# Kernel tuning notes

Hardware: AMD Instinct MI355X
Metric: run time of the kernel (lower is better)

## Reference

```python
import jax, jax.numpy as jnp
import numpy as np

N = 100000   # nodes
E = 600000   # edges
F_IN = 128   # input feature dim
H = 256      # hidden_channels


def setup_inputs() -> dict:
    key = jax.random.key(0)
    ks = jax.random.split(key, 8)
    x = jax.random.normal(ks[0], (N, F_IN), dtype=jnp.float32)
    edge_index = jax.random.randint(ks[1], (2, E), 0, N, dtype=jnp.int64)
    # SAGEConv params: out = lin_l(mean_agg) + lin_r(x_root); bias only on lin_l (PyG default)
    s1 = 1.0 / np.sqrt(F_IN)
    s2 = 1.0 / np.sqrt(H)
    Wl1 = jax.random.uniform(ks[2], (F_IN, H), jnp.float32, -s1, s1)
    Wr1 = jax.random.uniform(ks[3], (F_IN, H), jnp.float32, -s1, s1)
    b1 = jnp.zeros((H,), jnp.float32)
    Wl2 = jax.random.uniform(ks[4], (H, H), jnp.float32, -s2, s2)
    Wr2 = jax.random.uniform(ks[5], (H, H), jnp.float32, -s2, s2)
    b2 = jnp.zeros((H,), jnp.float32)
    return {"x": x, "edge_index": edge_index, "Wl1": Wl1, "Wr1": Wr1, "b1": b1,
            "Wl2": Wl2, "Wr2": Wr2, "b2": b2}


def _sage_conv(h, src, dst, Wl, Wr, b):
    # mean aggregation of source-node features at destination nodes
    msg = h[src]                                             # [E, d]
    agg = jax.ops.segment_sum(msg, dst, num_segments=N)      # [N, d]
    cnt = jax.ops.segment_sum(jnp.ones((src.shape[0],), h.dtype), dst, num_segments=N)
    agg = agg / jnp.maximum(cnt, 1.0)[:, None]
    return agg @ Wl + b + h @ Wr


def reference(x, edge_index, Wl1, Wr1, b1, Wl2, Wr2, b2):
    src, dst = edge_index[0], edge_index[1]
    h = jax.nn.relu(_sage_conv(x, src, dst, Wl1, Wr1, b1))
    return _sage_conv(h, src, dst, Wl2, Wr2, b2)
```

## Files before the change

### kernel.cpp

```cpp
#include <hip/hip_runtime.h>

#define Nn 100000
#define Ee 600000
#define Fin 128
#define Hd  256
#define NB  ((Nn + 1023) / 1024)

typedef __attribute__((ext_vector_type(8))) short short8;
typedef __attribute__((ext_vector_type(4))) float floatx4;

__device__ __forceinline__ float bf2f(unsigned short h) {
    return __uint_as_float(((unsigned int)h) << 16);
}
__device__ __forceinline__ unsigned short f2bf(float f) {
    unsigned int u = __float_as_uint(f);
    u += 0x7FFFu + ((u >> 16) & 1u);
    return (unsigned short)(u >> 16);
}
__device__ __forceinline__ float loadf(const void* p, int i, int f32) {
    return f32 ? ((const float*)p)[i] : bf2f(((const unsigned short*)p)[i]);
}
__device__ __forceinline__ void gload_lds16(const void* g, void* lds) {
    __builtin_amdgcn_global_load_lds((const __attribute__((address_space(1))) void*)g,
                                     (__attribute__((address_space(3))) void*)lds,
                                     16, 0, 0);
}

__global__ void k_detect(const unsigned int* __restrict__ ei,
                         const unsigned short* __restrict__ xu,
                         int* __restrict__ flag) {
    if (blockIdx.x == 0 && threadIdx.x == 0) {
        int is64 = 1;
        for (int i = 1; i < 64; i += 2)
            if (ei[i] != 0u) { is64 = 0; break; }
        flag[0] = is64;
        int isf32 = 0;
        for (int i = 0; i < 512; i += 2) {
            unsigned e = (xu[i] >> 7) & 0xFFu;
            if (e >= 0xC0u) { isf32 = 1; break; }
        }
        flag[1] = isf32;
    }
}

__device__ __forceinline__ void get_edge(const int* __restrict__ ei, int is64, int e,
                                         int& s, int& d) {
    if (is64) { s = ei[2 * e]; d = ei[2 * (Ee + e)]; }
    else      { s = ei[e];     d = ei[Ee + e]; }
}

__global__ void k_zero(int* __restrict__ p, int n) {
    int i = blockIdx.x * 256 + threadIdx.x;
    if (i < n) p[i] = 0;
}

__global__ void k_convert(const void* __restrict__ x, unsigned short* __restrict__ xb,
                          const int* __restrict__ flag) {
    int i = (blockIdx.x * 256 + threadIdx.x) * 4;
    if (i >= Nn * Fin) return;
    if (flag[1]) {
        float4 v = ((const float4*)x)[i >> 2];
        ushort4 u;
        u.x = f2bf(v.x); u.y = f2bf(v.y); u.z = f2bf(v.z); u.w = f2bf(v.w);
        ((ushort4*)xb)[i >> 2] = u;
    } else {
        ((ushort4*)xb)[i >> 2] = ((const ushort4*)x)[i >> 2];
    }
}

__global__ void k_prep(const void* __restrict__ Wl1, const void* __restrict__ Wr1,
                       const void* __restrict__ Wl2, const void* __restrict__ Wr2,
                       unsigned short* __restrict__ Wt1, unsigned short* __restrict__ Wt2,
                       const int* __restrict__ flag) {
    int f32 = flag[1];
    int tid = blockIdx.x * 256 + threadIdx.x;
    if (tid < 256 * 256) {
        int n = tid >> 8, k = tid & 255;
        float v = (k < 128) ? loadf(Wl1, k * 256 + n, f32) : loadf(Wr1, (k - 128) * 256 + n, f32);
        Wt1[n * 256 + k] = f2bf(v);
    }
    int t2 = tid - 256 * 256;
    if (t2 >= 0 && t2 < 256 * 512) {
        int n = t2 >> 9, k = t2 & 511;
        float v = (k < 256) ? loadf(Wl2, k * 256 + n, f32) : loadf(Wr2, (k - 256) * 256 + n, f32);
        Wt2[n * 512 + k] = f2bf(v);
    }
}

__global__ void k_count(const int* __restrict__ ei, const int* __restrict__ flag,
                        int* __restrict__ cnt) {
    int e = blockIdx.x * 256 + threadIdx.x;
    if (e >= Ee) return;
    int is64 = flag[0], s, d;
    get_edge(ei, is64, e, s, d);
    atomicAdd(&cnt[d], 1);
}

__global__ void k_bsum(const int* __restrict__ cnt, int* __restrict__ bsum) {
    __shared__ int red[256];
    int b = blockIdx.x, t = threadIdx.x;
    int i = b * 1024 + t * 4;
    int s = 0;
    if (i + 3 < Nn) {
        int4 v = *reinterpret_cast<const int4*>(cnt + i);
        s = v.x + v.y + v.z + v.w;
    } else {
        for (int j = 0; j < 4; j++) if (i + j < Nn) s += cnt[i + j];
    }
    red[t] = s;
    __syncthreads();
    for (int off = 128; off > 0; off >>= 1) {
        if (t < off) red[t] += red[t + off];
        __syncthreads();
    }
    if (t == 0) bsum[b] = red[0];
}

__global__ void k_bscan(const int* __restrict__ bsum, int* __restrict__ bpre,
                        int* __restrict__ rowptr) {
    __shared__ int sc[128];
    int t = threadIdx.x;
    int v = (t < NB) ? bsum[t] : 0;
    sc[t] = v;
    __syncthreads();
    for (int off = 1; off < 128; off <<= 1) {
        int add = (t >= off) ? sc[t - off] : 0;
        __syncthreads();
        sc[t] += add;
        __syncthreads();
    }
    if (t < NB) bpre[t] = sc[t] - v;
    if (t == 127) rowptr[Nn] = sc[127];
}

__global__ void k_rowptr(const int* __restrict__ cnt, const int* __restrict__ bpre,
                         int* __restrict__ rowptr) {
    __shared__ int sc[256];
    int b = blockIdx.x, t = threadIdx.x;
    int i = b * 1024 + t * 4;
    int4 c = make_int4(0, 0, 0, 0);
    if (i + 3 < Nn) {
        c = *reinterpret_cast<const int4*>(cnt + i);
    } else {
        if (i     < Nn) c.x = cnt[i];
        if (i + 1 < Nn) c.y = cnt[i + 1];
        if (i + 2 < Nn) c.z = cnt[i + 2];
        if (i + 3 < Nn) c.w = cnt[i + 3];
    }
    int s = c.x + c.y + c.z + c.w;
    sc[t] = s;
    __syncthreads();
    for (int off = 1; off < 256; off <<= 1) {
        int add = (t >= off) ? sc[t - off] : 0;
        __syncthreads();
        sc[t] += add;
        __syncthreads();
    }
    int p = bpre[b] + sc[t] - s;
    int4 r;
    r.x = p;
    r.y = r.x + c.x;
    r.z = r.y + c.y;
    r.w = r.z + c.z;
    if (i + 3 < Nn) {
        *reinterpret_cast<int4*>(rowptr + i) = r;
    } else {
        if (i     < Nn) rowptr[i]     = r.x;
        if (i + 1 < Nn) rowptr[i + 1] = r.y;
        if (i + 2 < Nn) rowptr[i + 2] = r.z;
        if (i + 3 < Nn) rowptr[i + 3] = r.w;
    }
}

__global__ void k_fill(const int* __restrict__ ei, const int* __restrict__ flag,
                       const int* __restrict__ rowptr, int* __restrict__ cur,
                       int* __restrict__ srcl) {
    int e = blockIdx.x * 256 + threadIdx.x;
    if (e >= Ee) return;
    int is64 = flag[0], s, d;
    get_edge(ei, is64, e, s, d);
    int pos = atomicAdd(&cur[d], 1);
    srcl[rowptr[d] + pos] = s;
}

template <int F, int SIN, int SOUT>
__device__ __forceinline__ void agg_body(const unsigned short* __restrict__ X,
                                         unsigned short* __restrict__ O,
                                         const int* __restrict__ rowptr,
                                         const int* __restrict__ srcl) {
    int gw = (blockIdx.x * blockDim.x + threadIdx.x) >> 6;
    int lane = threadIdx.x & 63;
    if (gw >= Nn) return;
    int b = rowptr[gw], e = rowptr[gw + 1];
    constexpr int C = F / 64;
    float acc[C] = {};
    if (e > b) {
        int last = e - 1;
        for (int i = b; i < e; i += 4) {
            int sv[4];
            float w[4];
#pragma unroll
            for (int j = 0; j < 4; j++) {
                int id = i + j;
                sv[j] = srcl[id < last ? id : last];
                w[j] = (id < e) ? 1.f : 0.f;
            }
            if constexpr (C == 2) {
                ushort2 u[4];
#pragma unroll
                for (int j = 0; j < 4; j++)
                    u[j] = *reinterpret_cast<const ushort2*>(X + (size_t)sv[j] * SIN + lane * 2);
#pragma unroll
                for (int j = 0; j < 4; j++) {
                    acc[0] = fmaf(w[j], bf2f(u[j].x), acc[0]);
                    acc[1] = fmaf(w[j], bf2f(u[j].y), acc[1]);
                }
            } else {
                ushort4 u[4];
#pragma unroll
                for (int j = 0; j < 4; j++)
                    u[j] = *reinterpret_cast<const ushort4*>(X + (size_t)sv[j] * SIN + lane * 4);
#pragma unroll
                for (int j = 0; j < 4; j++) {
                    acc[0] = fmaf(w[j], bf2f(u[j].x), acc[0]);
                    acc[1] = fmaf(w[j], bf2f(u[j].y), acc[1]);
                    acc[2] = fmaf(w[j], bf2f(u[j].z), acc[2]);
                    acc[3] = fmaf(w[j], bf2f(u[j].w), acc[3]);
                }
            }
        }
    }
    float inv = 1.f / (float)max(e - b, 1);
    unsigned short* op = O + (size_t)gw * SOUT + lane * C;
    if constexpr (C == 2) {
        ushort2 u; u.x = f2bf(acc[0] * inv); u.y = f2bf(acc[1] * inv);
        *reinterpret_cast<ushort2*>(op) = u;
    } else {
        ushort4 u;
        u.x = f2bf(acc[0] * inv); u.y = f2bf(acc[1] * inv);
        u.z = f2bf(acc[2] * inv); u.w = f2bf(acc[3] * inv);
        *reinterpret_cast<ushort4*>(op) = u;
    }
}

__global__ void k_agg1(const unsigned short* __restrict__ xb, unsigned short* __restrict__ agg1,
                       const int* __restrict__ rowptr, const int* __restrict__ srcl) {
    agg_body<Fin, Fin, Fin>(xb, agg1, rowptr, srcl);
}

__global__ void k_agg2(const int* __restrict__ rowptr, const int* __restrict__ srcl,
                       const int* __restrict__ flag, unsigned short* __restrict__ acat_ws,
                       void* __restrict__ out) {
    unsigned short* Acat = flag[1] ? (unsigned short*)out : acat_ws;
    agg_body<Hd, 512, 512>(Acat + 256, Acat, rowptr, srcl);
}

template <int KT, int K1, int S1, int S2>
__device__ __forceinline__ void gemm_core_lds(const unsigned short* __restrict__ A1,
                                              const unsigned short* __restrict__ A2,
                                              const unsigned short* __restrict__ Wt,
                                              floatx4 (&acc)[4][4],
                                              unsigned short* sA, unsigned short* sB,
                                              int m_base) {
    const int tid = threadIdx.x;
    const int lane = tid & 63, wid = tid >> 6;
    const int wm = wid & 1, wn = wid >> 1;
    const int quad = lane >> 4, l16 = lane & 15;
    const int n_base = wn * 64;
    const int rs = tid >> 3;
    const int cs = tid & 7;

    for (int kb = 0; kb < KT; kb += 64) {
        __syncthreads();
#pragma unroll
        for (int i = 0; i < 2; i++) {
            int r = i * 64 + rs;
            int gk = kb + ((cs ^ (r & 7)) << 3);
            int m = m_base + r; if (m >= Nn) m = Nn - 1;
            const unsigned short* gp = (gk < K1)
                ? A1 + (size_t)m * S1 + gk
                : A2 + (size_t)m * S2 + (gk - K1);
            gload_lds16(gp, sA + i * 4096 + wid * 512);
        }
#pragma unroll
        for (int i = 0; i < 4; i++) {
            int n = i * 64 + rs;
            int gk = kb + ((cs ^ (n & 7)) << 3);
            gload_lds16(Wt + (size_t)n * KT + gk, sB + i * 4096 + wid * 512);
        }
        __syncthreads();
#pragma unroll
        for (int ks = 0; ks < 64; ks += 32) {
            short8 a[4], b[4];
            int q = (ks >> 3) + quad;
#pragma unroll
            for (int mt = 0; mt < 4; mt++) {
                int r = wm * 64 + mt * 16 + l16;
                a[mt] = *reinterpret_cast<const short8*>(
                    sA + r * 64 + ((q ^ (l16 & 7)) << 3));
            }
#pragma unroll
            for (int nt = 0; nt < 4; nt++) {
                int n = n_base + nt * 16 + l16;
                b[nt] = *reinterpret_cast<const short8*>(
                    sB + n * 64 + ((q ^ (l16 & 7)) << 3));
            }
#pragma unroll
            for (int mt = 0; mt < 4; mt++)
#pragma unroll
                for (int nt = 0; nt < 4; nt++)
                    acc[mt][nt] = __builtin_amdgcn_mfma_f32_16x16x32_bf16(a[mt], b[nt], acc[mt][nt], 0, 0, 0);
        }
    }
}

__global__ __launch_bounds__(512) void k_gemm1(const unsigned short* __restrict__ agg1,
                                               const unsigned short* __restrict__ xb,
                                               const unsigned short* __restrict__ Wt1,
                                               const void* __restrict__ bias,
                                               const int* __restrict__ flag,
                                               unsigned short* __restrict__ acat_ws,
                                               void* __restrict__ out) {
    __shared__ unsigned short sA[8192];
    __shared__ unsigned short sB[16384];
    int f32 = flag[1];
    unsigned short* Acat = f32 ? (unsigned short*)out : acat_ws;
    int wid = threadIdx.x >> 6, lane = threadIdx.x & 63;
    int wm = wid & 1, wn = wid >> 1;
    int quad = lane >> 4, l16 = lane & 15;
    int m_base = blockIdx.x * 128;
    floatx4 acc[4][4] = {};
    gemm_core_lds<256, 128, 128, 128>(agg1, xb, Wt1, acc, sA, sB, m_base);
#pragma unroll
    for (int nt = 0; nt < 4; nt++) {
        int n = wn * 64 + nt * 16 + l16;
        float bv = loadf(bias, n, f32);
#pragma unroll
        for (int mt = 0; mt < 4; mt++) {
#pragma unroll
            for (int r = 0; r < 4; r++) {
                int m = m_base + wm * 64 + mt * 16 + quad * 4 + r;
                if (m < Nn) {
                    float v = acc[mt][nt][r] + bv;
                    v = v > 0.f ? v : 0.f;
                    Acat[(size_t)m * 512 + 256 + n] = f2bf(v);
                }
            }
        }
    }
}

__global__ __launch_bounds__(512) void k_gemm2(const unsigned short* __restrict__ Wt2,
                                               const void* __restrict__ bias,
                                               const int* __restrict__ flag,
                                               unsigned short* __restrict__ acat_ws,
                                               void* __restrict__ out) {
    __shared__ unsigned short sA[8192];
    __shared__ unsigned short sB[16384];
    int f32 = flag[1];
    unsigned short* Acat = f32 ? (unsigned short*)out : acat_ws;
    int wid = threadIdx.x >> 6, lane = threadIdx.x & 63;
    int wm = wid & 1, wn = wid >> 1;
    int quad = lane >> 4, l16 = lane & 15;
    int m_base = blockIdx.x * 128;
    floatx4 acc[4][4] = {};
    gemm_core_lds<512, 256, 512, 512>(Acat, Acat + 256, Wt2, acc, sA, sB, m_base);
    __syncthreads();
#pragma unroll
    for (int nt = 0; nt < 4; nt++) {
        int n = wn * 64 + nt * 16 + l16;
        float bv = loadf(bias, n, f32);
#pragma unroll
        for (int mt = 0; mt < 4; mt++) {
#pragma unroll
            for (int r = 0; r < 4; r++) {
                int m = m_base + wm * 64 + mt * 16 + quad * 4 + r;
                if (m < Nn) {
                    float v = acc[mt][nt][r] + bv;
                    if (f32) ((float*)out)[(size_t)m * Hd + n] = v;
                    else     ((unsigned short*)out)[(size_t)m * Hd + n] = f2bf(v);
                }
            }
        }
    }
}

extern "C" void kernel_launch(void* const* d_in, const int* in_sizes, int n_in,
                              void* d_out, int out_size, void* d_ws, size_t ws_size,
                              hipStream_t stream) {
    const void* x   = d_in[0];
    const int*  ei  = (const int*)d_in[1];
    const void* Wl1 = d_in[2];
    const void* Wr1 = d_in[3];
    const void* b1  = d_in[4];
    const void* Wl2 = d_in[5];
    const void* Wr2 = d_in[6];
    const void* b2  = d_in[7];

    char* ws = (char*)d_ws;
    size_t off_cnt    = 0;
    size_t off_cur    = off_cnt + (size_t)Nn * 4;
    size_t off_rowptr = off_cur + (size_t)Nn * 4;
    size_t off_srcl   = off_rowptr + (size_t)(Nn + 4) * 4;
    size_t off_flag   = off_srcl + (size_t)Ee * 4;
    size_t off_bsum   = ((off_flag + 8 + 255) / 256) * 256;
    size_t off_bpre   = off_bsum + 128 * 4;
    size_t off_wt1    = off_bpre + 128 * 4;
    size_t off_wt2    = off_wt1 + 256 * 256 * 2;
    size_t off_xb     = off_wt2 + 256 * 512 * 2;
    size_t off_agg1   = off_xb + (size_t)Nn * Fin * 2;
    size_t off_acat   = off_agg1 + (size_t)Nn * Fin * 2;

    int*            cnt     = (int*)(ws + off_cnt);
    int*            cur     = (int*)(ws + off_cur);
    int*            rowptr  = (int*)(ws + off_rowptr);
    int*            srcl    = (int*)(ws + off_srcl);
    int*            flag    = (int*)(ws + off_flag);
    int*            bsum    = (int*)(ws + off_bsum);
    int*            bpre    = (int*)(ws + off_bpre);
    unsigned short* Wt1     = (unsigned short*)(ws + off_wt1);
    unsigned short* Wt2     = (unsigned short*)(ws + off_wt2);
    unsigned short* xb      = (unsigned short*)(ws + off_xb);
    unsigned short* agg1    = (unsigned short*)(ws + off_agg1);
    unsigned short* acat_ws = (unsigned short*)(ws + off_acat);

    k_detect<<<1, 64, 0, stream>>>((const unsigned int*)ei, (const unsigned short*)x, flag);
    k_zero<<<(2 * Nn + 255) / 256, 256, 0, stream>>>(cnt, 2 * Nn);
    k_convert<<<(Nn * Fin / 4 + 255) / 256, 256, 0, stream>>>(x, xb, flag);
    k_prep<<<768, 256, 0, stream>>>(Wl1, Wr1, Wl2, Wr2, Wt1, Wt2, flag);

    int eb = (Ee + 255) / 256;
    k_count<<<eb, 256, 0, stream>>>(ei, flag, cnt);
    k_bsum<<<NB, 256, 0, stream>>>(cnt, bsum);
    k_bscan<<<1, 128, 0, stream>>>(bsum, bpre, rowptr);
    k_rowptr<<<NB, 256, 0, stream>>>(cnt, bpre, rowptr);
    k_fill<<<eb, 256, 0, stream>>>(ei, flag, rowptr, cur, srcl);

    int ab = (Nn * 64 + 255) / 256;
    int gx = (Nn + 127) / 128;

    k_agg1<<<ab, 256, 0, stream>>>(xb, agg1, rowptr, srcl);
    k_gemm1<<<gx, 512, 0, stream>>>(agg1, xb, Wt1, b1, flag, acat_ws, d_out);
    k_agg2<<<ab, 256, 0, stream>>>(rowptr, srcl, flag, acat_ws, d_out);
    k_gemm2<<<gx, 512, 0, stream>>>(Wt2, b2, flag, acat_ws, d_out);
}
```

Before: 406.5 us.

## Double-buffer GEMM LDS tiles to overlap global loads with MFMA compute

Result: slower. 425.5 us (+4.7%).

```diff
diff --git a/kernel.cpp b/kernel.cpp
--- a/kernel.cpp
+++ b/kernel.cpp
@@ -249,69 +249,89 @@
 }
 
 __global__ void k_agg2(const int* __restrict__ rowptr, const int* __restrict__ srcl,
-                       const int* __restrict__ flag, unsigned short* __restrict__ acat_ws,
-                       void* __restrict__ out) {
-    unsigned short* Acat = flag[1] ? (unsigned short*)out : acat_ws;
-    agg_body<Hd, 512, 512>(Acat + 256, Acat, rowptr, srcl);
+                       unsigned short* __restrict__ acat_ws) {
+    agg_body<Hd, 512, 512>(acat_ws + 256, acat_ws, rowptr, srcl);
 }
 
 template <int KT, int K1, int S1, int S2>
-__device__ __forceinline__ void gemm_core_lds(const unsigned short* __restrict__ A1,
-                                              const unsigned short* __restrict__ A2,
-                                              const unsigned short* __restrict__ Wt,
-                                              floatx4 (&acc)[4][4],
-                                              unsigned short* sA, unsigned short* sB,
-                                              int m_base) {
+__device__ __forceinline__ void gemm_core_pipe(const unsigned short* __restrict__ A1,
+                                               const unsigned short* __restrict__ A2,
+                                               const unsigned short* __restrict__ Wt,
+                                               floatx4 (&acc)[4][4],
+                                               unsigned short* sA, unsigned short* sB,
+                                               int m_base) {
     const int tid = threadIdx.x;
     const int lane = tid & 63, wid = tid >> 6;
     const int wm = wid & 1, wn = wid >> 1;
     const int quad = lane >> 4, l16 = lane & 15;
-    const int n_base = wn * 64;
-    const int rs = tid >> 3;
-    const int cs = tid & 7;
-
-    for (int kb = 0; kb < KT; kb += 64) {
-        __syncthreads();
-#pragma unroll
-        for (int i = 0; i < 2; i++) {
-            int r = i * 64 + rs;
-            int gk = kb + ((cs ^ (r & 7)) << 3);
-            int m = m_base + r; if (m >= Nn) m = Nn - 1;
-            const unsigned short* gp = (gk < K1)
-                ? A1 + (size_t)m * S1 + gk
-                : A2 + (size_t)m * S2 + (gk - K1);
-            gload_lds16(gp, sA + i * 4096 + wid * 512);
-        }
-#pragma unroll
-        for (int i = 0; i < 4; i++) {
-            int n = i * 64 + rs;
-            int gk = kb + ((cs ^ (n & 7)) << 3);
-            gload_lds16(Wt + (size_t)n * KT + gk, sB + i * 4096 + wid * 512);
-        }
-        __syncthreads();
-#pragma unroll
-        for (int ks = 0; ks < 64; ks += 32) {
-            short8 a[4], b[4];
-            int q = (ks >> 3) + quad;
-#pragma unroll
-            for (int mt = 0; mt < 4; mt++) {
-                int r = wm * 64 + mt * 16 + l16;
-                a[mt] = *reinterpret_cast<const short8*>(
-                    sA + r * 64 + ((q ^ (l16 & 7)) << 3));
-            }
-#pragma unroll
-            for (int nt = 0; nt < 4; nt++) {
-                int n = n_base + nt * 16 + l16;
-                b[nt] = *reinterpret_cast<const short8*>(
-                    sB + n * 64 + ((q ^ (l16 & 7)) << 3));
-            }
-#pragma unroll
-            for (int mt = 0; mt < 4; mt++)
-#pragma unroll
-                for (int nt = 0; nt < 4; nt++)
-                    acc[mt][nt] = __builtin_amdgcn_mfma_f32_16x16x32_bf16(a[mt], b[nt], acc[mt][nt], 0, 0, 0);
-        }
-    }
+    const int rs = tid >> 2, cs = tid & 3;
+    constexpr int NT = KT / 32;
+
+#define STAGE(t, buf)                                                              \
+    {                                                                              \
+        int kb_ = (t) * 32;                                                        \
+        {                                                                          \
+            int r_ = rs;                                                           \
+            int gk_ = kb_ + ((cs ^ ((r_ >> 1) & 3)) << 3);                         \
+            int m_ = m_base + r_; if (m_ >= Nn) m_ = Nn - 1;                       \
+            const unsigned short* gp_ = (gk_ < K1)                                 \
+                ? A1 + (size_t)m_ * S1 + gk_                                       \
+                : A2 + (size_t)m_ * S2 + (gk_ - K1);                               \
+            gload_lds16(gp_, sA + (buf) * 4096 + wid * 512);                       \
+        }                                                                          \
+        _Pragma("unroll")                                                          \
+        for (int i_ = 0; i_ < 2; i_++) {                                           \
+            int n_ = i_ * 128 + rs;                                                \
+            int gk_ = kb_ + ((cs ^ ((n_ >> 1) & 3)) << 3);                         \
+            gload_lds16(Wt + (size_t)n_ * KT + gk_,                                \
+                        sB + (buf) * 8192 + i_ * 4096 + wid * 512);                \
+        }                                                                          \
+    }
+
+#define COMPUTE(buf)                                                               \
+    {                                                                              \
+        short8 a_[4], b_[4];                                                       \
+        _Pragma("unroll")                                                          \
+        for (int mt_ = 0; mt_ < 4; mt_++) {                                        \
+            int r_ = wm * 64 + mt_ * 16 + l16;                                     \
+            a_[mt_] = *reinterpret_cast<const short8*>(                            \
+                sA + (buf) * 4096 + r_ * 32 + ((quad ^ ((r_ >> 1) & 3)) << 3));    \
+        }                                                                          \
+        _Pragma("unroll")                                                          \
+        for (int nt_ = 0; nt_ < 4; nt_++) {                                        \
+            int n_ = wn * 64 + nt_ * 16 + l16;                                     \
+            b_[nt_] = *reinterpret_cast<const short8*>(                            \
+                sB + (buf) * 8192 + n_ * 32 + ((quad ^ ((n_ >> 1) & 3)) << 3));    \
+        }                                                                          \
+        _Pragma("unroll")                                                          \
+        for (int mt_ = 0; mt_ < 4; mt_++)                                          \
+            _Pragma("unroll")                                                      \
+            for (int nt_ = 0; nt_ < 4; nt_++)                                      \
+                acc[mt_][nt_] = __builtin_amdgcn_mfma_f32_16x16x32_bf16(           \
+                    a_[mt_], b_[nt_], acc[mt_][nt_], 0, 0, 0);                     \
+    }
+
+    STAGE(0, 0)
+#pragma unroll
+    for (int t = 0; t < NT - 1; t++) {
+        STAGE(t + 1, (t + 1) & 1)
+        asm volatile("s_waitcnt vmcnt(3)" ::: "memory");
+        __builtin_amdgcn_sched_barrier(0);
+        __builtin_amdgcn_s_barrier();
+        __builtin_amdgcn_sched_barrier(0);
+        COMPUTE(t & 1)
+        __builtin_amdgcn_sched_barrier(0);
+        asm volatile("s_waitcnt lgkmcnt(0)" ::: "memory");
+        __builtin_amdgcn_s_barrier();
+        __builtin_amdgcn_sched_barrier(0);
+    }
+    asm volatile("s_waitcnt vmcnt(0)" ::: "memory");
+    __builtin_amdgcn_sched_barrier(0);
+    __builtin_amdgcn_s_barrier();
+    __builtin_amdgcn_sched_barrier(0);
+    COMPUTE((NT - 1) & 1)
+#undef STAGE
+#undef COMPUTE
 }
 
 __global__ __launch_bounds__(512) void k_gemm1(const unsigned short* __restrict__ agg1,
@@ -319,18 +339,16 @@
                                                const unsigned short* __restrict__ Wt1,
                                                const void* __restrict__ bias,
                                                const int* __restrict__ flag,
-                                               unsigned short* __restrict__ acat_ws,
-                                               void* __restrict__ out) {
+                                               unsigned short* __restrict__ acat_ws) {
     __shared__ unsigned short sA[8192];
     __shared__ unsigned short sB[16384];
     int f32 = flag[1];
-    unsigned short* Acat = f32 ? (unsigned short*)out : acat_ws;
     int wid = threadIdx.x >> 6, lane = threadIdx.x & 63;
     int wm = wid & 1, wn = wid >> 1;
     int quad = lane >> 4, l16 = lane & 15;
     int m_base = blockIdx.x * 128;
     floatx4 acc[4][4] = {};
-    gemm_core_lds<256, 128, 128, 128>(agg1, xb, Wt1, acc, sA, sB, m_base);
+    gemm_core_pipe<256, 128, 128, 128>(agg1, xb, Wt1, acc, sA, sB, m_base);
 #pragma unroll
     for (int nt = 0; nt < 4; nt++) {
         int n = wn * 64 + nt * 16 + l16;
@@ -343,7 +361,7 @@
                 if (m < Nn) {
                     float v = acc[mt][nt][r] + bv;
                     v = v > 0.f ? v : 0.f;
-                    Acat[(size_t)m * 512 + 256 + n] = f2bf(v);
+                    acat_ws[(size_t)m * 512 + 256 + n] = f2bf(v);
                 }
             }
         }
@@ -353,19 +371,17 @@
 __global__ __launch_bounds__(512) void k_gemm2(const unsigned short* __restrict__ Wt2,
                                                const void* __restrict__ bias,
                                                const int* __restrict__ flag,
-                                               unsigned short* __restrict__ acat_ws,
+                                               const unsigned short* __restrict__ acat_ws,
                                                void* __restrict__ out) {
     __shared__ unsigned short sA[8192];
     __shared__ unsigned short sB[16384];
     int f32 = flag[1];
-    unsigned short* Acat = f32 ? (unsigned short*)out : acat_ws;
     int wid = threadIdx.x >> 6, lane = threadIdx.x & 63;
     int wm = wid & 1, wn = wid >> 1;
     int quad = lane >> 4, l16 = lane & 15;
     int m_base = blockIdx.x * 128;
     floatx4 acc[4][4] = {};
-    gemm_core_lds<512, 256, 512, 512>(Acat, Acat + 256, Wt2, acc, sA, sB, m_base);
-    __syncthreads();
+    gemm_core_pipe<512, 256, 512, 512>(acat_ws, acat_ws + 256, Wt2, acc, sA, sB, m_base);
 #pragma unroll
     for (int nt = 0; nt < 4; nt++) {
         int n = wn * 64 + nt * 16 + l16;
@@ -440,7 +456,7 @@
     int gx = (Nn + 127) / 128;
 
     k_agg1<<<ab, 256, 0, stream>>>(xb, agg1, rowptr, srcl);
-    k_gemm1<<<gx, 512, 0, stream>>>(agg1, xb, Wt1, b1, flag, acat_ws, d_out);
-    k_agg2<<<ab, 256, 0, stream>>>(rowptr, srcl, flag, acat_ws, d_out);
+    k_gemm1<<<gx, 512, 0, stream>>>(agg1, xb, Wt1, b1, flag, acat_ws);
+    k_agg2<<<ab, 256, 0, stream>>>(rowptr, srcl, acat_ws);
     k_gemm2<<<gx, 512, 0, stream>>>(Wt2, b2, flag, acat_ws, d_out);
 }
```
